# Kernel optimization log

Hardware: AMD Instinct MI355X
Metric: run time of the kernel (lower is better)

The kernel has to match this reference:

```python
import math
import jax, jax.numpy as jnp
import numpy as np

L = 16
LOG2T = 19
T = 1 << LOG2T
F = 2
N_MIN = 16
N_MAX = 2048
N_PTS = 1048576

# intended geometric growth factor (source has a parenthesization bug)
_B = math.exp((math.log(N_MAX) - math.log(N_MIN)) / (L - 1))
RESOLUTIONS = [int(math.floor(N_MIN * (_B ** i))) for i in range(L)]

# 8 corner offsets of a voxel, [8, 3]
_OFFS_NP = np.stack(np.meshgrid([0, 1], [0, 1], [0, 1], indexing='ij'), -1).reshape(8, 3)
# spatial hash primes from Instant-NGP
_PRIMES_NP = np.array([1, 2654435761, 805459861], dtype=np.uint32)


def setup_inputs() -> dict:
    key = jax.random.key(0)
    k1, k2 = jax.random.split(key)
    x = jax.random.uniform(k1, (N_PTS, 3), dtype=jnp.float32)  # positions in [0,1)
    table = jax.random.normal(k2, (L, T, F), dtype=jnp.float32) * 1e-4
    return {"x": x, "table": table}


def _encode(x, table):
    offs_i = jnp.asarray(_OFFS_NP, dtype=jnp.uint32)          # [8,3]
    offs_f = jnp.asarray(_OFFS_NP, dtype=x.dtype)             # [8,3]
    primes = jnp.asarray(_PRIMES_NP)                          # [3] uint32
    mask = jnp.uint32(T - 1)
    outs = []
    for lvl in range(L):
        res = RESOLUTIONS[lvl]
        xs = x * res                                           # [N,3]
        x0 = jnp.floor(xs)
        w = xs - x0                                            # [N,3] trilerp weights
        # corner integer coords, [N,8,3]
        c = x0.astype(jnp.uint32)[:, None, :] + offs_i[None]
        # spatial hash: xor of coord*prime, masked to T (T is a power of 2)
        hp = c * primes                                        # uint32 wraparound mul
        h = (hp[..., 0] ^ hp[..., 1] ^ hp[..., 2]) & mask      # [N,8]
        feats = table[lvl][h.astype(jnp.int32)]                # [N,8,F] gather
        # trilinear weights: prod over dims of (w if corner==1 else 1-w)
        wts = jnp.prod(jnp.where(offs_f[None] == 1.0, w[:, None, :], 1.0 - w[:, None, :]), axis=-1)  # [N,8]
        outs.append(jnp.einsum('nc,ncf->nf', wts, feats))      # [N,F]
    return jnp.concatenate(outs, axis=-1)                      # [N, L*F]


def reference(x, table):
    return _encode(x, table)
```

## Files before the change

### kernel.cpp

```cpp
#include <hip/hip_runtime.h>
#include <cmath>

#define NPTS   1048576
#define NLVL   16
#define NLOW   5
#define T      (1u << 19)
#define TMASK  (T - 1u)
#define P1     2654435761u
#define P2     805459861u

typedef float v2f __attribute__((ext_vector_type(2)));
typedef float v4f __attribute__((ext_vector_type(4)));

struct Corners { uint32_t h[8]; float wt[8]; };

__device__ __forceinline__ Corners mk_corners(float px, float py, float pz, float rf) {
    Corners cc;
    const float xs0 = px * rf, xs1 = py * rf, xs2 = pz * rf;
    const float f0 = floorf(xs0), f1 = floorf(xs1), f2 = floorf(xs2);
    const float w0 = xs0 - f0, w1 = xs1 - f1, w2 = xs2 - f2;
    const uint32_t i0 = (uint32_t)f0, i1 = (uint32_t)f1, i2 = (uint32_t)f2;
    const uint32_t A0 = i0,      A1 = i0 + 1u;
    const uint32_t B0 = i1 * P1, B1 = B0 + P1;
    const uint32_t C0 = i2 * P2, C1 = C0 + P2;
    cc.h[0] = (A0 ^ B0 ^ C0) & TMASK;  cc.h[1] = (A0 ^ B0 ^ C1) & TMASK;
    cc.h[2] = (A0 ^ B1 ^ C0) & TMASK;  cc.h[3] = (A0 ^ B1 ^ C1) & TMASK;
    cc.h[4] = (A1 ^ B0 ^ C0) & TMASK;  cc.h[5] = (A1 ^ B0 ^ C1) & TMASK;
    cc.h[6] = (A1 ^ B1 ^ C0) & TMASK;  cc.h[7] = (A1 ^ B1 ^ C1) & TMASK;
    const float u0 = 1.0f - w0, u1 = 1.0f - w1, u2 = 1.0f - w2;
    cc.wt[0] = (u0 * u1) * u2;  cc.wt[1] = (u0 * u1) * w2;
    cc.wt[2] = (u0 * w1) * u2;  cc.wt[3] = (u0 * w1) * w2;
    cc.wt[4] = (w0 * u1) * u2;  cc.wt[5] = (w0 * u1) * w2;
    cc.wt[6] = (w0 * w1) * u2;  cc.wt[7] = (w0 * w1) * w2;
    return cc;
}

__global__ __launch_bounds__(256) void hashgrid_lvl1(
    const float* __restrict__ x,
    const float* __restrict__ tb,
    float* __restrict__ wsl,
    float rf)
{
    const int n = blockIdx.x * 256 + threadIdx.x;
    const float px = __builtin_nontemporal_load(x + 3 * (size_t)n + 0);
    const float py = __builtin_nontemporal_load(x + 3 * (size_t)n + 1);
    const float pz = __builtin_nontemporal_load(x + 3 * (size_t)n + 2);
    const Corners cc = mk_corners(px, py, pz, rf);
    float a0 = 0.f, a1 = 0.f;
#pragma unroll
    for (int c = 0; c < 8; ++c) {
        const float2 g = *(const float2*)(tb + 2 * (size_t)cc.h[c]);
        a0 += cc.wt[c] * g.x;
        a1 += cc.wt[c] * g.y;
    }
    v2f r; r.x = a0; r.y = a1;
    __builtin_nontemporal_store(r, (v2f*)(wsl + (size_t)n * 2));
}

__global__ __launch_bounds__(256) void hashgrid_lvl4pt(
    const float* __restrict__ x,
    const float* __restrict__ tb,
    float* __restrict__ wsl,
    float rf)
{
    const int t = blockIdx.x * 256 + threadIdx.x;

    float a0[4], a1[4];
#pragma unroll
    for (int p = 0; p < 4; ++p) {
        const int n = t + p * (NPTS / 4);
        const float px = __builtin_nontemporal_load(x + 3 * (size_t)n + 0);
        const float py = __builtin_nontemporal_load(x + 3 * (size_t)n + 1);
        const float pz = __builtin_nontemporal_load(x + 3 * (size_t)n + 2);
        const Corners cc = mk_corners(px, py, pz, rf);
        float s0 = 0.f, s1 = 0.f;
#pragma unroll
        for (int c = 0; c < 8; ++c) {
            const float2 g = *(const float2*)(tb + 2 * (size_t)cc.h[c]);
            s0 += cc.wt[c] * g.x;
            s1 += cc.wt[c] * g.y;
        }
        a0[p] = s0; a1[p] = s1;
    }
#pragma unroll
    for (int p = 0; p < 4; ++p) {
        const int n = t + p * (NPTS / 4);
        v2f r; r.x = a0[p]; r.y = a1[p];
        __builtin_nontemporal_store(r, (v2f*)(wsl + (size_t)n * 2));
    }
}

__global__ __launch_bounds__(256) void hashgrid_transpose(
    const float* __restrict__ ws,
    float* __restrict__ out)
{
    const int n = blockIdx.x * 256 + threadIdx.x;
    float acc[2 * NLVL];
#pragma unroll
    for (int l = 0; l < NLVL; ++l) {
        const v2f g = __builtin_nontemporal_load(
            (const v2f*)(ws + ((size_t)l << 21) + (size_t)n * 2));
        acc[2 * l + 0] = g.x;
        acc[2 * l + 1] = g.y;
    }
    v4f* op = (v4f*)(out + (size_t)n * 32);
#pragma unroll
    for (int k = 0; k < 8; ++k) {
        v4f v; v.x = acc[4*k]; v.y = acc[4*k+1]; v.z = acc[4*k+2]; v.w = acc[4*k+3];
        op[k] = v;
    }
}

__global__ __launch_bounds__(256) void hashgrid_lvl_direct(
    const float* __restrict__ x,
    const float* __restrict__ tb,
    float* __restrict__ outl,
    float rf)
{
    const int n = blockIdx.x * 256 + threadIdx.x;
    const float px = __builtin_nontemporal_load(x + 3 * (size_t)n + 0);
    const float py = __builtin_nontemporal_load(x + 3 * (size_t)n + 1);
    const float pz = __builtin_nontemporal_load(x + 3 * (size_t)n + 2);
    const Corners cc = mk_corners(px, py, pz, rf);
    float a0 = 0.f, a1 = 0.f;
#pragma unroll
    for (int c = 0; c < 8; ++c) {
        const float2 g = *(const float2*)(tb + 2 * (size_t)cc.h[c]);
        a0 += cc.wt[c] * g.x;
        a1 += cc.wt[c] * g.y;
    }
    outl[(size_t)n * 32 + 0] = a0;
    outl[(size_t)n * 32 + 1] = a1;
}

extern "C" void kernel_launch(void* const* d_in, const int* in_sizes, int n_in,
                              void* d_out, int out_size, void* d_ws, size_t ws_size,
                              hipStream_t stream) {
    const float* x     = (const float*)d_in[0];
    const float* table = (const float*)d_in[1];
    float* out         = (float*)d_out;
    float* ws          = (float*)d_ws;

    double (*volatile p_log)(double)          = log;
    double (*volatile p_exp)(double)          = exp;
    double (*volatile p_pow)(double, double)  = pow;
    double (*volatile p_floor)(double)        = floor;

    const double b = p_exp((p_log(2048.0) - p_log(16.0)) / 15.0);
    float rf[NLVL];
    for (int l = 0; l < NLVL; ++l)
        rf[l] = (float)(int)p_floor(16.0 * p_pow(b, (double)l));

    const bool use_ws = ws_size >= (size_t)NLVL * NPTS * 2 * sizeof(float);

    if (!use_ws) {
        for (int l = 0; l < NLVL; ++l)
            hashgrid_lvl_direct<<<NPTS / 256, 256, 0, stream>>>(
                x, table + ((size_t)l << 20), out + 2 * l, rf[l]);
        return;
    }

    for (int l = NLOW; l < NLVL; ++l) {
        hashgrid_lvl4pt<<<NPTS / 1024, 256, 0, stream>>>(
            x, table + ((size_t)l << 20), ws + ((size_t)l << 21), rf[l]);
    }
    for (int l = 0; l < NLOW; ++l) {
        hashgrid_lvl1<<<NPTS / 256, 256, 0, stream>>>(
            x, table + ((size_t)l << 20), ws + ((size_t)l << 21), rf[l]);
    }
    hashgrid_transpose<<<NPTS / 256, 256, 0, stream>>>(ws, out);
}
```

Measured before the change: 623.7 us.

## Store per-level workspace in fp16 and process two adjacent points per thread

Per-level intermediate results are now written to the workspace as half precision and widened back to fp32 in the transpose kernel, halving workspace write and read traffic. The high-level kernel is replaced by one handling two consecutive points per thread, with vectorized coalesced loads of positions. The cost is reduced precision of the encoded features from fp16 rounding, and less memory-level parallelism per thread than the prior four-point version.

```diff
diff --git a/kernel.cpp b/kernel.cpp
--- a/kernel.cpp
+++ b/kernel.cpp
@@ -9,8 +9,10 @@
 #define P1     2654435761u
 #define P2     805459861u
 
-typedef float v2f __attribute__((ext_vector_type(2)));
-typedef float v4f __attribute__((ext_vector_type(4)));
+typedef float    v2f __attribute__((ext_vector_type(2)));
+typedef float    v4f __attribute__((ext_vector_type(4)));
+typedef _Float16 v2h __attribute__((ext_vector_type(2)));
+typedef _Float16 v4h __attribute__((ext_vector_type(4)));
 
 struct Corners { uint32_t h[8]; float wt[8]; };
 
@@ -35,10 +37,39 @@
     return cc;
 }
 
+__global__ __launch_bounds__(256) void hashgrid_lvl2pt(
+    const float* __restrict__ x,
+    const float* __restrict__ tb,
+    _Float16* __restrict__ wsl,
+    float rf)
+{
+    const int t = blockIdx.x * 256 + threadIdx.x;
+
+    const v2f q0 = __builtin_nontemporal_load((const v2f*)(x + 6 * (size_t)t + 0));
+    const v2f q1 = __builtin_nontemporal_load((const v2f*)(x + 6 * (size_t)t + 2));
+    const v2f q2 = __builtin_nontemporal_load((const v2f*)(x + 6 * (size_t)t + 4));
+
+    const Corners c0 = mk_corners(q0.x, q0.y, q1.x, rf);
+    const Corners c1 = mk_corners(q1.y, q2.x, q2.y, rf);
+
+    float a00 = 0.f, a01 = 0.f, a10 = 0.f, a11 = 0.f;
+#pragma unroll
+    for (int c = 0; c < 8; ++c) {
+        const float2 g0 = *(const float2*)(tb + 2 * (size_t)c0.h[c]);
+        const float2 g1 = *(const float2*)(tb + 2 * (size_t)c1.h[c]);
+        a00 += c0.wt[c] * g0.x;  a01 += c0.wt[c] * g0.y;
+        a10 += c1.wt[c] * g1.x;  a11 += c1.wt[c] * g1.y;
+    }
+    v4h r;
+    r.x = (_Float16)a00;  r.y = (_Float16)a01;
+    r.z = (_Float16)a10;  r.w = (_Float16)a11;
+    __builtin_nontemporal_store(r, (v4h*)(wsl + 4 * (size_t)t));
+}
+
 __global__ __launch_bounds__(256) void hashgrid_lvl1(
     const float* __restrict__ x,
     const float* __restrict__ tb,
-    float* __restrict__ wsl,
+    _Float16* __restrict__ wsl,
     float rf)
 {
     const int n = blockIdx.x * 256 + threadIdx.x;
@@ -53,55 +84,22 @@
         a0 += cc.wt[c] * g.x;
         a1 += cc.wt[c] * g.y;
     }
-    v2f r; r.x = a0; r.y = a1;
-    __builtin_nontemporal_store(r, (v2f*)(wsl + (size_t)n * 2));
-}
-
-__global__ __launch_bounds__(256) void hashgrid_lvl4pt(
-    const float* __restrict__ x,
-    const float* __restrict__ tb,
-    float* __restrict__ wsl,
-    float rf)
-{
-    const int t = blockIdx.x * 256 + threadIdx.x;
-
-    float a0[4], a1[4];
-#pragma unroll
-    for (int p = 0; p < 4; ++p) {
-        const int n = t + p * (NPTS / 4);
-        const float px = __builtin_nontemporal_load(x + 3 * (size_t)n + 0);
-        const float py = __builtin_nontemporal_load(x + 3 * (size_t)n + 1);
-        const float pz = __builtin_nontemporal_load(x + 3 * (size_t)n + 2);
-        const Corners cc = mk_corners(px, py, pz, rf);
-        float s0 = 0.f, s1 = 0.f;
-#pragma unroll
-        for (int c = 0; c < 8; ++c) {
-            const float2 g = *(const float2*)(tb + 2 * (size_t)cc.h[c]);
-            s0 += cc.wt[c] * g.x;
-            s1 += cc.wt[c] * g.y;
-        }
-        a0[p] = s0; a1[p] = s1;
-    }
-#pragma unroll
-    for (int p = 0; p < 4; ++p) {
-        const int n = t + p * (NPTS / 4);
-        v2f r; r.x = a0[p]; r.y = a1[p];
-        __builtin_nontemporal_store(r, (v2f*)(wsl + (size_t)n * 2));
-    }
+    v2h r; r.x = (_Float16)a0; r.y = (_Float16)a1;
+    __builtin_nontemporal_store(r, (v2h*)(wsl + 2 * (size_t)n));
 }
 
 __global__ __launch_bounds__(256) void hashgrid_transpose(
-    const float* __restrict__ ws,
+    const _Float16* __restrict__ ws,
     float* __restrict__ out)
 {
     const int n = blockIdx.x * 256 + threadIdx.x;
     float acc[2 * NLVL];
 #pragma unroll
     for (int l = 0; l < NLVL; ++l) {
-        const v2f g = __builtin_nontemporal_load(
-            (const v2f*)(ws + ((size_t)l << 21) + (size_t)n * 2));
-        acc[2 * l + 0] = g.x;
-        acc[2 * l + 1] = g.y;
+        const v2h g = __builtin_nontemporal_load(
+            (const v2h*)(ws + ((size_t)l << 21) + (size_t)n * 2));
+        acc[2 * l + 0] = (float)g.x;
+        acc[2 * l + 1] = (float)g.y;
     }
     v4f* op = (v4f*)(out + (size_t)n * 32);
 #pragma unroll
@@ -139,7 +137,7 @@
     const float* x     = (const float*)d_in[0];
     const float* table = (const float*)d_in[1];
     float* out         = (float*)d_out;
-    float* ws          = (float*)d_ws;
+    _Float16* ws       = (_Float16*)d_ws;
 
     double (*volatile p_log)(double)          = log;
     double (*volatile p_exp)(double)          = exp;
@@ -151,7 +149,7 @@
     for (int l = 0; l < NLVL; ++l)
         rf[l] = (float)(int)p_floor(16.0 * p_pow(b, (double)l));
 
-    const bool use_ws = ws_size >= (size_t)NLVL * NPTS * 2 * sizeof(float);
+    const bool use_ws = ws_size >= (size_t)NLVL * NPTS * 2 * sizeof(_Float16);
 
     if (!use_ws) {
         for (int l = 0; l < NLVL; ++l)
@@ -161,7 +159,7 @@
     }
 
     for (int l = NLOW; l < NLVL; ++l) {
-        hashgrid_lvl4pt<<<NPTS / 1024, 256, 0, stream>>>(
+        hashgrid_lvl2pt<<<NPTS / 512, 256, 0, stream>>>(
             x, table + ((size_t)l << 20), ws + ((size_t)l << 21), rf[l]);
     }
     for (int l = 0; l < NLOW; ++l) {
```

Result: faster. 560.3 us (-10.2%).
